# Optimization experiments

Measured on AMD Instinct MI355X. Metric: run time of the kernel, lower is better.

The kernel has to match this reference:

```python
import jax, jax.numpy as jnp
import numpy as np

N_BLOCKS = 8
BLOCK = 512
HIDDEN = N_BLOCKS * BLOCK  # 4096


def setup_inputs() -> dict:
    key = jax.random.key(0)
    k1, k2 = jax.random.split(key)
    x = jax.random.normal(k1, (4, 4096, HIDDEN), dtype=jnp.float32)
    # per-sub-transform matrices (what trans.get_matrix(inv_t) would return)
    blocks = jax.random.normal(k2, (N_BLOCKS, BLOCK, BLOCK), dtype=jnp.float32)
    return {"x": x, "blocks": blocks}


def reference(x, blocks):
    # Original: matrix = block_diag(*blocks); out = x.reshape(-1, H) @ matrix
    # Block-diagonal structure means each hidden slice of size BLOCK only
    # multiplies its own block -> grouped GEMM, identical math, no zeros.
    init_shape = x.shape
    xr = x.reshape(-1, N_BLOCKS, BLOCK)  # [tokens, k, b]
    out = jnp.einsum("nkb,kbc->nkc", xr, blocks)
    return out.reshape(init_shape)
```

## Files before the change

### kernel.cpp

```cpp
#include <hip/hip_runtime.h>
#include <stdint.h>


#define HID 4096
#define KD  512
#define NKB 8
#define BM  128
#define BN  128
#define BK  32
#define MTILES 128
#define NWG   (MTILES * NKB * 4)
#define ASTRIDE 40

typedef __attribute__((ext_vector_type(4))) float    f32x4;
typedef __attribute__((ext_vector_type(8))) short    s16x8;
typedef __attribute__((ext_vector_type(4))) uint32_t u32x4;

__device__ uint16_t g_bt[(size_t)NKB * KD * KD];

__device__ __forceinline__ void async_copy16(const void* g, void* l) {
  __builtin_amdgcn_global_load_lds((const __attribute__((address_space(1))) void*)g,
                                   (__attribute__((address_space(3))) void*)l,
                                   16, 0, 0);
}

__device__ __forceinline__ uint16_t f2bf_rne(float f) {
  uint32_t u = __float_as_uint(f);
  u += 0x7fffu + ((u >> 16) & 1u);
  return (uint16_t)(u >> 16);
}

__global__ void convert_blocks_k(const float* __restrict__ blocks) {
  __shared__ float tile[32][33];
  const int kb = blockIdx.z;
  const int c0 = blockIdx.x * 32;
  const int b0 = blockIdx.y * 32;
  const int tx = threadIdx.x;
  const int ty = threadIdx.y;
  const float* src = blocks + ((size_t)kb * KD + b0) * KD + c0;
#pragma unroll
  for (int i = 0; i < 4; ++i) {
    const int r = ty + i * 8;
    tile[r][tx] = src[(size_t)r * KD + tx];
  }
  __syncthreads();
  uint16_t* dst = g_bt + ((size_t)kb * KD + c0) * KD + b0;
#pragma unroll
  for (int i = 0; i < 4; ++i) {
    const int r = ty + i * 8;
    dst[(size_t)r * KD + tx] = f2bf_rne(tile[tx][r]);
  }
}

__global__ void grouped_gemm_k(const float* __restrict__ x, float* __restrict__ out) {
  __shared__ uint16_t lA[BM * ASTRIDE];
  __shared__ uint16_t lB[BN * BK];

  const int tid = threadIdx.x;

  const int pid = blockIdx.x;
  const int wg  = (pid & 7) * (NWG / 8) + (pid >> 3);
  const int nt  =  wg       & 3;
  const int kb  = (wg >> 2) & 7;
  const int mt  =  wg >> 5;

  const int wave = tid >> 6;
  const int lane = tid & 63;
  const int ln   = lane & 15;
  const int qd   = lane >> 4;
  const int wm   = (wave & 1) * 64;
  const int wn   = (wave >> 1) * 64;

  const int am = tid >> 1;
  const int ah = tid & 1;
  const float* aptr = x + (size_t)(mt * BM + am) * HID + kb * KD + ah * 16;
  uint16_t* awr = lA + am * ASTRIDE + ah * 16;

  const int bn0 = tid >> 2;
  const int bs0 = (tid & 3) ^ (bn0 & 3) ^ ((bn0 >> 2) & 3);
  const int p1  = tid + 256;
  const int bn1 = p1 >> 2;
  const int bs1 = (p1 & 3) ^ (bn1 & 3) ^ ((bn1 >> 2) & 3);
  const uint16_t* bsrc0 = g_bt + (size_t)(kb * KD + nt * BN + bn0) * KD + bs0 * 8;
  const uint16_t* bsrc1 = g_bt + (size_t)(kb * KD + nt * BN + bn1) * KD + bs1 * 8;
  uint16_t* bdst0 = lB + tid * 8;
  uint16_t* bdst1 = lB + p1 * 8;

  const int sw = (ln & 3) ^ ((ln >> 2) & 3);
  const uint16_t* ard = lA + (wm + ln) * ASTRIDE + qd * 8;
  const uint16_t* brd = lB + ((wn + ln) * 4 + (qd ^ sw)) * 8;

  f32x4 acc[4][4];
#pragma unroll
  for (int mi = 0; mi < 4; ++mi)
#pragma unroll
    for (int ni = 0; ni < 4; ++ni)
      acc[mi][ni] = (f32x4){0.f, 0.f, 0.f, 0.f};

  for (int kk = 0; kk < KD / BK; ++kk) {
    const int k0 = kk * BK;
    const f32x4 a0 = *(const f32x4*)(aptr + k0);
    const f32x4 a1 = *(const f32x4*)(aptr + k0 + 4);
    const f32x4 a2 = *(const f32x4*)(aptr + k0 + 8);
    const f32x4 a3 = *(const f32x4*)(aptr + k0 + 12);

    __syncthreads();

    async_copy16(bsrc0 + k0, bdst0);
    async_copy16(bsrc1 + k0, bdst1);

    u32x4 w0, w1;
    w0.x = __builtin_amdgcn_perm(__float_as_uint(a0.y), __float_as_uint(a0.x), 0x07060302u);
    w0.y = __builtin_amdgcn_perm(__float_as_uint(a0.w), __float_as_uint(a0.z), 0x07060302u);
    w0.z = __builtin_amdgcn_perm(__float_as_uint(a1.y), __float_as_uint(a1.x), 0x07060302u);
    w0.w = __builtin_amdgcn_perm(__float_as_uint(a1.w), __float_as_uint(a1.z), 0x07060302u);
    w1.x = __builtin_amdgcn_perm(__float_as_uint(a2.y), __float_as_uint(a2.x), 0x07060302u);
    w1.y = __builtin_amdgcn_perm(__float_as_uint(a2.w), __float_as_uint(a2.z), 0x07060302u);
    w1.z = __builtin_amdgcn_perm(__float_as_uint(a3.y), __float_as_uint(a3.x), 0x07060302u);
    w1.w = __builtin_amdgcn_perm(__float_as_uint(a3.w), __float_as_uint(a3.z), 0x07060302u);
    *(u32x4*)(awr)     = w0;
    *(u32x4*)(awr + 8) = w1;

    __syncthreads();

    s16x8 af[4], bf[4];
#pragma unroll
    for (int mi = 0; mi < 4; ++mi) af[mi] = *(const s16x8*)(ard + mi * (16 * ASTRIDE));
#pragma unroll
    for (int ni = 0; ni < 4; ++ni) bf[ni] = *(const s16x8*)(brd + ni * (16 * 32));
#pragma unroll
    for (int mi = 0; mi < 4; ++mi)
#pragma unroll
      for (int ni = 0; ni < 4; ++ni)
        acc[mi][ni] = __builtin_amdgcn_mfma_f32_16x16x32_bf16(bf[ni], af[mi], acc[mi][ni], 0, 0, 0);
  }

  const int mbase = mt * BM + wm;
  const int nbase = kb * KD + nt * BN + wn + qd * 4;
#pragma unroll
  for (int mi = 0; mi < 4; ++mi) {
    float* orow = out + (size_t)(mbase + mi * 16 + ln) * HID + nbase;
#pragma unroll
    for (int ni = 0; ni < 4; ++ni)
      __builtin_nontemporal_store(acc[mi][ni], (f32x4*)(orow + ni * 16));
  }
}

extern "C" void kernel_launch(void* const* d_in, const int* in_sizes, int n_in,
                              void* d_out, int out_size, void* d_ws, size_t ws_size,
                              hipStream_t stream) {
  const float* x      = (const float*)d_in[0];
  const float* blocks = (const float*)d_in[1];
  float* out = (float*)d_out;
  (void)d_ws; (void)ws_size; (void)in_sizes; (void)n_in; (void)out_size;

  convert_blocks_k<<<dim3(16, 16, 8), dim3(32, 8, 1), 0, stream>>>(blocks);
  grouped_gemm_k<<<dim3(NWG, 1, 1), dim3(256, 1, 1), 0, stream>>>(x, out);
}
```

Measured before the change: 545.1 us.

## Double-buffer LDS tiles to overlap next-tile loads with MFMA compute

Splits the A and B shared-memory tiles into two buffers and restructures the K loop as a prologue plus a software pipeline. Global loads and async B copies for tile k+1 are issued before the MFMAs on tile k. The bf16 pack of A is stored into the other buffer after compute, which removes one barrier per iteration. This doubles LDS use, which may reduce occupancy, and holds the prefetched A registers across the MFMA block.

```diff
diff --git a/kernel.cpp b/kernel.cpp
--- a/kernel.cpp
+++ b/kernel.cpp
@@ -8,6 +8,7 @@
 #define BM  128
 #define BN  128
 #define BK  32
+#define NKK (KD / BK)
 #define MTILES 128
 #define NWG   (MTILES * NKB * 4)
 #define ASTRIDE 40
@@ -53,8 +54,8 @@
 }
 
 __global__ void grouped_gemm_k(const float* __restrict__ x, float* __restrict__ out) {
-  __shared__ uint16_t lA[BM * ASTRIDE];
-  __shared__ uint16_t lB[BN * BK];
+  __shared__ uint16_t lA[2][BM * ASTRIDE];
+  __shared__ uint16_t lB[2][BN * BK];
 
   const int tid = threadIdx.x;
 
@@ -74,7 +75,7 @@
   const int am = tid >> 1;
   const int ah = tid & 1;
   const float* aptr = x + (size_t)(mt * BM + am) * HID + kb * KD + ah * 16;
-  uint16_t* awr = lA + am * ASTRIDE + ah * 16;
+  const int awo = am * ASTRIDE + ah * 16;
 
   const int bn0 = tid >> 2;
   const int bs0 = (tid & 3) ^ (bn0 & 3) ^ ((bn0 >> 2) & 3);
@@ -83,12 +84,12 @@
   const int bs1 = (p1 & 3) ^ (bn1 & 3) ^ ((bn1 >> 2) & 3);
   const uint16_t* bsrc0 = g_bt + (size_t)(kb * KD + nt * BN + bn0) * KD + bs0 * 8;
   const uint16_t* bsrc1 = g_bt + (size_t)(kb * KD + nt * BN + bn1) * KD + bs1 * 8;
-  uint16_t* bdst0 = lB + tid * 8;
-  uint16_t* bdst1 = lB + p1 * 8;
+  const int bdo0 = tid * 8;
+  const int bdo1 = p1 * 8;
 
-  const int sw = (ln & 3) ^ ((ln >> 2) & 3);
-  const uint16_t* ard = lA + (wm + ln) * ASTRIDE + qd * 8;
-  const uint16_t* brd = lB + ((wn + ln) * 4 + (qd ^ sw)) * 8;
+  const int sw   = (ln & 3) ^ ((ln >> 2) & 3);
+  const int ardo = (wm + ln) * ASTRIDE + qd * 8;
+  const int brdo = ((wn + ln) * 4 + (qd ^ sw)) * 8;
 
   f32x4 acc[4][4];
 #pragma unroll
@@ -97,18 +98,13 @@
     for (int ni = 0; ni < 4; ++ni)
       acc[mi][ni] = (f32x4){0.f, 0.f, 0.f, 0.f};
 
-  for (int kk = 0; kk < KD / BK; ++kk) {
-    const int k0 = kk * BK;
-    const f32x4 a0 = *(const f32x4*)(aptr + k0);
-    const f32x4 a1 = *(const f32x4*)(aptr + k0 + 4);
-    const f32x4 a2 = *(const f32x4*)(aptr + k0 + 8);
-    const f32x4 a3 = *(const f32x4*)(aptr + k0 + 12);
-
-    __syncthreads();
-
-    async_copy16(bsrc0 + k0, bdst0);
-    async_copy16(bsrc1 + k0, bdst1);
-
+  {
+    const f32x4 a0 = *(const f32x4*)(aptr);
+    const f32x4 a1 = *(const f32x4*)(aptr + 4);
+    const f32x4 a2 = *(const f32x4*)(aptr + 8);
+    const f32x4 a3 = *(const f32x4*)(aptr + 12);
+    async_copy16(bsrc0, &lB[0][bdo0]);
+    async_copy16(bsrc1, &lB[0][bdo1]);
     u32x4 w0, w1;
     w0.x = __builtin_amdgcn_perm(__float_as_uint(a0.y), __float_as_uint(a0.x), 0x07060302u);
     w0.y = __builtin_amdgcn_perm(__float_as_uint(a0.w), __float_as_uint(a0.z), 0x07060302u);
@@ -118,21 +114,52 @@
     w1.y = __builtin_amdgcn_perm(__float_as_uint(a2.w), __float_as_uint(a2.z), 0x07060302u);
     w1.z = __builtin_amdgcn_perm(__float_as_uint(a3.y), __float_as_uint(a3.x), 0x07060302u);
     w1.w = __builtin_amdgcn_perm(__float_as_uint(a3.w), __float_as_uint(a3.z), 0x07060302u);
-    *(u32x4*)(awr)     = w0;
-    *(u32x4*)(awr + 8) = w1;
+    *(u32x4*)(&lA[0][awo])     = w0;
+    *(u32x4*)(&lA[0][awo + 8]) = w1;
+  }
+  __syncthreads();
 
-    __syncthreads();
+#pragma unroll
+  for (int kk = 0; kk < NKK; ++kk) {
+    const int p = kk & 1;
+    const int q = p ^ 1;
+
+    f32x4 a0, a1, a2, a3;
+    if (kk + 1 < NKK) {
+      const int k1 = (kk + 1) * BK;
+      async_copy16(bsrc0 + k1, &lB[q][bdo0]);
+      async_copy16(bsrc1 + k1, &lB[q][bdo1]);
+      a0 = *(const f32x4*)(aptr + k1);
+      a1 = *(const f32x4*)(aptr + k1 + 4);
+      a2 = *(const f32x4*)(aptr + k1 + 8);
+      a3 = *(const f32x4*)(aptr + k1 + 12);
+    }
 
     s16x8 af[4], bf[4];
 #pragma unroll
-    for (int mi = 0; mi < 4; ++mi) af[mi] = *(const s16x8*)(ard + mi * (16 * ASTRIDE));
+    for (int mi = 0; mi < 4; ++mi) af[mi] = *(const s16x8*)(&lA[p][ardo + mi * (16 * ASTRIDE)]);
 #pragma unroll
-    for (int ni = 0; ni < 4; ++ni) bf[ni] = *(const s16x8*)(brd + ni * (16 * 32));
+    for (int ni = 0; ni < 4; ++ni) bf[ni] = *(const s16x8*)(&lB[p][brdo + ni * (16 * 32)]);
 #pragma unroll
     for (int mi = 0; mi < 4; ++mi)
 #pragma unroll
       for (int ni = 0; ni < 4; ++ni)
         acc[mi][ni] = __builtin_amdgcn_mfma_f32_16x16x32_bf16(bf[ni], af[mi], acc[mi][ni], 0, 0, 0);
+
+    if (kk + 1 < NKK) {
+      u32x4 w0, w1;
+      w0.x = __builtin_amdgcn_perm(__float_as_uint(a0.y), __float_as_uint(a0.x), 0x07060302u);
+      w0.y = __builtin_amdgcn_perm(__float_as_uint(a0.w), __float_as_uint(a0.z), 0x07060302u);
+      w0.z = __builtin_amdgcn_perm(__float_as_uint(a1.y), __float_as_uint(a1.x), 0x07060302u);
+      w0.w = __builtin_amdgcn_perm(__float_as_uint(a1.w), __float_as_uint(a1.z), 0x07060302u);
+      w1.x = __builtin_amdgcn_perm(__float_as_uint(a2.y), __float_as_uint(a2.x), 0x07060302u);
+      w1.y = __builtin_amdgcn_perm(__float_as_uint(a2.w), __float_as_uint(a2.z), 0x07060302u);
+      w1.z = __builtin_amdgcn_perm(__float_as_uint(a3.y), __float_as_uint(a3.x), 0x07060302u);
+      w1.w = __builtin_amdgcn_perm(__float_as_uint(a3.w), __float_as_uint(a3.z), 0x07060302u);
+      *(u32x4*)(&lA[q][awo])     = w0;
+      *(u32x4*)(&lA[q][awo + 8]) = w1;
+      __syncthreads();
+    }
   }
 
   const int mbase = mt * BM + wm;
```

Measured after the change: 543.8 us. Within noise of the previous version (-0.2%).

## Keep full B panel in LDS, load A directly into registers with prefetch

Applied to the files above, without the earlier changes.

Each workgroup now loads its whole 64x512 bf16 B panel into LDS once, with an XOR swizzle, before the loop. A is no longer staged through LDS: each lane reads its fp32 A fragments straight from global memory, converts them to bf16 in registers, and double-buffers them to prefetch the next k-step. This removes the per-iteration barriers and the LDS round trip for A. The tile shape becomes 256x64 with 512 threads. Each A element is now read by more workgroups (8 N-tiles instead of 4), and the uncoalesced per-lane global A loads could raise memory traffic.

```diff
diff --git a/kernel.cpp b/kernel.cpp
--- a/kernel.cpp
+++ b/kernel.cpp
@@ -5,12 +5,13 @@
 #define HID 4096
 #define KD  512
 #define NKB 8
-#define BM  128
-#define BN  128
+#define BM  256
+#define BN  64
 #define BK  32
-#define MTILES 128
-#define NWG   (MTILES * NKB * 4)
-#define ASTRIDE 40
+#define NKK (KD / BK)
+#define MTILES 64
+#define NNT    8
+#define NWG   (MTILES * NKB * NNT)
 
 typedef __attribute__((ext_vector_type(4))) float    f32x4;
 typedef __attribute__((ext_vector_type(8))) short    s16x8;
@@ -52,86 +53,91 @@
   }
 }
 
-__global__ void grouped_gemm_k(const float* __restrict__ x, float* __restrict__ out) {
-  __shared__ uint16_t lA[BM * ASTRIDE];
-  __shared__ uint16_t lB[BN * BK];
+__global__ __launch_bounds__(512, 2)
+void grouped_gemm_k(const float* __restrict__ x, float* __restrict__ out) {
+  __shared__ uint16_t lB[BN * KD];
 
   const int tid = threadIdx.x;
 
   const int pid = blockIdx.x;
   const int wg  = (pid & 7) * (NWG / 8) + (pid >> 3);
-  const int nt  =  wg       & 3;
-  const int kb  = (wg >> 2) & 7;
-  const int mt  =  wg >> 5;
+  const int nt  =  wg       & 7;
+  const int kb  = (wg >> 3) & 7;
+  const int mt  =  wg >> 6;
 
   const int wave = tid >> 6;
   const int lane = tid & 63;
   const int ln   = lane & 15;
   const int qd   = lane >> 4;
-  const int wm   = (wave & 1) * 64;
-  const int wn   = (wave >> 1) * 64;
+  const int wm   = (wave & 3) * 64;
+  const int wn   = (wave >> 2) * 32;
 
-  const int am = tid >> 1;
-  const int ah = tid & 1;
-  const float* aptr = x + (size_t)(mt * BM + am) * HID + kb * KD + ah * 16;
-  uint16_t* awr = lA + am * ASTRIDE + ah * 16;
+  const uint8_t* gb = (const uint8_t*)g_bt + ((size_t)(kb * KD + nt * BN)) * KD * 2;
+#pragma unroll
+  for (int i = 0; i < 8; ++i) {
+    const int L    = (tid + 512 * i) * 16;
+    const int n    = L >> 10;
+    const int koff = L & 1023;
+    async_copy16(gb + (size_t)n * 1024 + (koff ^ ((n & 7) << 4)),
+                 (uint8_t*)lB + L);
+  }
 
-  const int bn0 = tid >> 2;
-  const int bs0 = (tid & 3) ^ (bn0 & 3) ^ ((bn0 >> 2) & 3);
-  const int p1  = tid + 256;
-  const int bn1 = p1 >> 2;
-  const int bs1 = (p1 & 3) ^ (bn1 & 3) ^ ((bn1 >> 2) & 3);
-  const uint16_t* bsrc0 = g_bt + (size_t)(kb * KD + nt * BN + bn0) * KD + bs0 * 8;
-  const uint16_t* bsrc1 = g_bt + (size_t)(kb * KD + nt * BN + bn1) * KD + bs1 * 8;
-  uint16_t* bdst0 = lB + tid * 8;
-  uint16_t* bdst1 = lB + p1 * 8;
+  const float* aptr = x + (size_t)(mt * BM + wm + ln) * HID + kb * KD + qd * 8;
 
-  const int sw = (ln & 3) ^ ((ln >> 2) & 3);
-  const uint16_t* ard = lA + (wm + ln) * ASTRIDE + qd * 8;
-  const uint16_t* brd = lB + ((wn + ln) * 4 + (qd ^ sw)) * 8;
-
-  f32x4 acc[4][4];
+  f32x4 acc[4][2];
 #pragma unroll
   for (int mi = 0; mi < 4; ++mi)
 #pragma unroll
-    for (int ni = 0; ni < 4; ++ni)
+    for (int ni = 0; ni < 2; ++ni)
       acc[mi][ni] = (f32x4){0.f, 0.f, 0.f, 0.f};
 
-  for (int kk = 0; kk < KD / BK; ++kk) {
-    const int k0 = kk * BK;
-    const f32x4 a0 = *(const f32x4*)(aptr + k0);
-    const f32x4 a1 = *(const f32x4*)(aptr + k0 + 4);
-    const f32x4 a2 = *(const f32x4*)(aptr + k0 + 8);
-    const f32x4 a3 = *(const f32x4*)(aptr + k0 + 12);
+  f32x4 ab[2][8];
+#pragma unroll
+  for (int mi = 0; mi < 4; ++mi) {
+    const float* p = aptr + (size_t)mi * 16 * HID;
+    ab[0][mi * 2]     = *(const f32x4*)(p);
+    ab[0][mi * 2 + 1] = *(const f32x4*)(p + 4);
+  }
 
-    __syncthreads();
+  __syncthreads();
 
-    async_copy16(bsrc0 + k0, bdst0);
-    async_copy16(bsrc1 + k0, bdst1);
+  const int rowbase = wn + ln;
+#pragma unroll
+  for (int kk = 0; kk < NKK; ++kk) {
+    const int cb = kk & 1, nb = cb ^ 1;
+    const int k1 = ((kk + 1) & (NKK - 1)) * BK;
+#pragma unroll
+    for (int mi = 0; mi < 4; ++mi) {
+      const float* p = aptr + (size_t)mi * 16 * HID + k1;
+      ab[nb][mi * 2]     = *(const f32x4*)(p);
+      ab[nb][mi * 2 + 1] = *(const f32x4*)(p + 4);
+    }
 
-    u32x4 w0, w1;
-    w0.x = __builtin_amdgcn_perm(__float_as_uint(a0.y), __float_as_uint(a0.x), 0x07060302u);
-    w0.y = __builtin_amdgcn_perm(__float_as_uint(a0.w), __float_as_uint(a0.z), 0x07060302u);
-    w0.z = __builtin_amdgcn_perm(__float_as_uint(a1.y), __float_as_uint(a1.x), 0x07060302u);
-    w0.w = __builtin_amdgcn_perm(__float_as_uint(a1.w), __float_as_uint(a1.z), 0x07060302u);
-    w1.x = __builtin_amdgcn_perm(__float_as_uint(a2.y), __float_as_uint(a2.x), 0x07060302u);
-    w1.y = __builtin_amdgcn_perm(__float_as_uint(a2.w), __float_as_uint(a2.z), 0x07060302u);
-    w1.z = __builtin_amdgcn_perm(__float_as_uint(a3.y), __float_as_uint(a3.x), 0x07060302u);
-    w1.w = __builtin_amdgcn_perm(__float_as_uint(a3.w), __float_as_uint(a3.z), 0x07060302u);
-    *(u32x4*)(awr)     = w0;
-    *(u32x4*)(awr + 8) = w1;
+    s16x8 af[4];
+#pragma unroll
+    for (int mi = 0; mi < 4; ++mi) {
+      const f32x4 lo = ab[cb][mi * 2];
+      const f32x4 hi = ab[cb][mi * 2 + 1];
+      u32x4 w;
+      w.x = __builtin_amdgcn_perm(__float_as_uint(lo.y), __float_as_uint(lo.x), 0x07060302u);
+      w.y = __builtin_amdgcn_perm(__float_as_uint(lo.w), __float_as_uint(lo.z), 0x07060302u);
+      w.z = __builtin_amdgcn_perm(__float_as_uint(hi.y), __float_as_uint(hi.x), 0x07060302u);
+      w.w = __builtin_amdgcn_perm(__float_as_uint(hi.w), __float_as_uint(hi.z), 0x07060302u);
+      af[mi] = __builtin_bit_cast(s16x8, w);
+    }
 
-    __syncthreads();
+    s16x8 bf[2];
+#pragma unroll
+    for (int ni = 0; ni < 2; ++ni) {
+      const int row = rowbase + ni * 16;
+      const int off = (kk * 64 + qd * 16) ^ ((row & 7) << 4);
+      bf[ni] = *(const s16x8*)((const uint8_t*)lB + (size_t)row * 1024 + off);
+    }
 
-    s16x8 af[4], bf[4];
-#pragma unroll
-    for (int mi = 0; mi < 4; ++mi) af[mi] = *(const s16x8*)(ard + mi * (16 * ASTRIDE));
-#pragma unroll
-    for (int ni = 0; ni < 4; ++ni) bf[ni] = *(const s16x8*)(brd + ni * (16 * 32));
 #pragma unroll
     for (int mi = 0; mi < 4; ++mi)
 #pragma unroll
-      for (int ni = 0; ni < 4; ++ni)
+      for (int ni = 0; ni < 2; ++ni)
         acc[mi][ni] = __builtin_amdgcn_mfma_f32_16x16x32_bf16(bf[ni], af[mi], acc[mi][ni], 0, 0, 0);
   }
 
@@ -141,7 +147,7 @@
   for (int mi = 0; mi < 4; ++mi) {
     float* orow = out + (size_t)(mbase + mi * 16 + ln) * HID + nbase;
 #pragma unroll
-    for (int ni = 0; ni < 4; ++ni)
+    for (int ni = 0; ni < 2; ++ni)
       __builtin_nontemporal_store(acc[mi][ni], (f32x4*)(orow + ni * 16));
   }
 }
@@ -155,5 +161,5 @@
   (void)d_ws; (void)ws_size; (void)in_sizes; (void)n_in; (void)out_size;
 
   convert_blocks_k<<<dim3(16, 16, 8), dim3(32, 8, 1), 0, stream>>>(blocks);
-  grouped_gemm_k<<<dim3(NWG, 1, 1), dim3(256, 1, 1), 0, stream>>>(x, out);
+  grouped_gemm_k<<<dim3(NWG, 1, 1), dim3(512, 1, 1), 0, stream>>>(x, out);
 }
```

After: 836.3 us. +53.4%, slower.
